# Performance work log

Measured on AMD Instinct MI355X. Metric: run time of the kernel, lower is better.

The kernel has to match this reference:

```python
import jax, jax.numpy as jnp
import numpy as np
import math

K = 8
MOMENTUM = 0.999


def _gelu(x):
    c = math.sqrt(2.0 / math.pi)
    return 0.5 * x * (1.0 + jnp.tanh(c * (x + 0.044715 * x ** 3)))


def _normalize(v, eps=1e-12):
    n = jnp.linalg.norm(v, axis=-1, keepdims=True)
    return v / jnp.maximum(n, eps)


def setup_inputs() -> dict:
    key = jax.random.key(0)
    k1, k2 = jax.random.split(key)
    B, T, D = 4, 4096, 2048
    x = jax.random.normal(k1, (B, T, D), dtype=jnp.float32)
    prototypes = _normalize(jax.random.normal(k2, (K, D), dtype=jnp.float32))
    log_tau = jnp.asarray(math.log(2.0), dtype=jnp.float32)
    log_blend = jnp.asarray(math.log(0.3 / 0.7), dtype=jnp.float32)
    return {"x": x, "prototypes": prototypes, "log_tau": log_tau, "log_blend": log_blend}


def reference(x, prototypes, log_tau, log_blend):
    tau = jnp.exp(log_tau)
    alpha = jax.nn.sigmoid(log_blend)
    B, T, D = x.shape
    x_flat = jax.lax.stop_gradient(x.reshape(-1, D))  # [N, D], detached

    P_norm = _normalize(prototypes)                  # [K, D]
    xn = _normalize(x_flat, eps=1e-8)                # [N, D]

    sims = jnp.clip(xn @ P_norm.T, -1.0, 1.0)        # [N, K]
    assignments = jnp.argmax(sims, axis=-1)          # [N]

    # masked per-cluster mean via segment-sum (vectorized over K)
    sums = jax.ops.segment_sum(x_flat, assignments, num_segments=K)       # [K, D]
    counts = jax.ops.segment_sum(jnp.ones((x_flat.shape[0],), x.dtype),
                                 assignments, num_segments=K)             # [K]
    has = (counts > 0)[:, None]
    centroids = jnp.where(has, sums / jnp.maximum(counts, 1.0)[:, None], prototypes)
    new_P = _normalize(centroids)

    P2 = MOMENTUM * prototypes + (1.0 - MOMENTUM) * new_P
    P2n = _normalize(P2, eps=1e-8)

    sims2 = jnp.clip(xn @ P2n.T, -1.0, 1.0)          # [N, K]
    dists = jnp.clip(1.0 - jnp.max(sims2, axis=-1), 0.0, 2.0)
    novelty = (1.0 - jnp.exp(-tau * dists)).reshape(B, T)

    scale = jnp.clip(1.0 - alpha + alpha * novelty[..., None], 0.1, 10.0)
    return _gelu(x * scale)
```

## Files before the change

### kernel.cpp

```cpp
#include <hip/hip_runtime.h>

#define N_TOK 16384
#define DDIM  2048
#define KC    8
#define CH1   32
#define TBA   4
#define TBF   4

typedef float nfloat4 __attribute__((ext_vector_type(4)));

__device__ __forceinline__ void nt_store4(const float4& v, float* p){
  nfloat4 nv; nv.x = v.x; nv.y = v.y; nv.z = v.z; nv.w = v.w;
  __builtin_nontemporal_store(nv, (nfloat4*)p);
}
__device__ __forceinline__ float4 nt_load4(const float* p){
  nfloat4 nv = __builtin_nontemporal_load((const nfloat4*)p);
  return make_float4(nv.x, nv.y, nv.z, nv.w);
}

__device__ __forceinline__ float wave_sum(float v){
  #pragma unroll
  for (int off = 32; off > 0; off >>= 1)
    v += __shfl_xor(v, off, 64);
  return v;
}

__device__ __forceinline__ float butterfly8(float v[8], int t){
  {
    const bool h = (t & 1);
    #pragma unroll
    for (int j = 0; j < 4; ++j){
      float s    = h ? v[j]   : v[j+4];
      float keep = h ? v[j+4] : v[j];
      v[j] = keep + __shfl_xor(s, 1, 64);
    }
  }
  {
    const bool h = (t & 2);
    #pragma unroll
    for (int j = 0; j < 2; ++j){
      float s    = h ? v[j]   : v[j+2];
      float keep = h ? v[j+2] : v[j];
      v[j] = keep + __shfl_xor(s, 2, 64);
    }
  }
  {
    const bool h = (t & 4);
    float s    = h ? v[0] : v[1];
    float keep = h ? v[1] : v[0];
    v[0] = keep + __shfl_xor(s, 4, 64);
  }
  v[0] += __shfl_xor(v[0], 8, 64);
  v[0] += __shfl_xor(v[0], 16, 64);
  v[0] += __shfl_xor(v[0], 32, 64);
  return v[0];
}

__device__ __forceinline__ float gelu_tanh(float v){
  const float c = 0.7978845608028654f;
  float tt = c * v * (1.0f + 0.044715f * v * v);
  float e  = __expf(2.0f * tt);
  float th = 1.0f - 2.0f / (e + 1.0f);
  return 0.5f * v * (1.0f + th);
}

__global__ __launch_bounds__(256, 2)
void k_assign(const float* __restrict__ x, const float* __restrict__ proto,
              float* __restrict__ psums, float* __restrict__ pcnts, int ntok)
{
  const int t = threadIdx.x;
  const int wave = t >> 6, lane = t & 63;
  const int d0 = 4*t, d1 = DDIM/2 + 4*t;
  const int kidx = ((lane&1)<<2) | (lane&2) | ((lane>>2)&1);

  __shared__ float rednorm[4*KC];
  __shared__ float red[TBA][4][KC];
  __shared__ float sInv[KC];
  __shared__ float sCnt[KC];
  __shared__ int   sAsg[TBA];

  float4 P0[KC], P1[KC];
  float4 acc0[KC], acc1[KC];
  #pragma unroll
  for (int k = 0; k < KC; ++k){
    P0[k] = *(const float4*)(proto + k*DDIM + d0);
    P1[k] = *(const float4*)(proto + k*DDIM + d1);
    acc0[k] = make_float4(0.f,0.f,0.f,0.f);
    acc1[k] = make_float4(0.f,0.f,0.f,0.f);
  }
  if (t < KC) sCnt[t] = 0.f;

  #pragma unroll
  for (int k = 0; k < KC; ++k){
    float ss = P0[k].x*P0[k].x + P0[k].y*P0[k].y + P0[k].z*P0[k].z + P0[k].w*P0[k].w
             + P1[k].x*P1[k].x + P1[k].y*P1[k].y + P1[k].z*P1[k].z + P1[k].w*P1[k].w;
    ss = wave_sum(ss);
    if (lane == 0) rednorm[wave*KC + k] = ss;
  }
  __syncthreads();
  if (t < KC){
    float ss = rednorm[t] + rednorm[KC + t] + rednorm[2*KC + t] + rednorm[3*KC + t];
    sInv[t] = 1.0f / fmaxf(sqrtf(ss), 1e-12f);
  }
  __syncthreads();

  const int stride = gridDim.x * TBA;
  float4 X0[TBA], X1[TBA], N0[TBA], N1[TBA];
  int tok0 = blockIdx.x * TBA;
  #pragma unroll
  for (int i = 0; i < TBA; ++i){
    int tk = tok0 + i;
    X0[i] = make_float4(0,0,0,0); X1[i] = make_float4(0,0,0,0);
    if (tk < ntok){
      X0[i] = *(const float4*)(x + (size_t)tk*DDIM + d0);
      X1[i] = *(const float4*)(x + (size_t)tk*DDIM + d1);
    }
  }

  for (; tok0 < ntok; tok0 += stride){
    const int ntok0 = tok0 + stride;
    #pragma unroll
    for (int i = 0; i < TBA; ++i){
      int tk = ntok0 + i;
      N0[i] = make_float4(0,0,0,0); N1[i] = make_float4(0,0,0,0);
      if (tk < ntok){
        N0[i] = *(const float4*)(x + (size_t)tk*DDIM + d0);
        N1[i] = *(const float4*)(x + (size_t)tk*DDIM + d1);
      }
    }
    #pragma unroll
    for (int i = 0; i < TBA; ++i){
      float v[KC];
      #pragma unroll
      for (int k = 0; k < KC; ++k){
        v[k] = X0[i].x*P0[k].x + X0[i].y*P0[k].y + X0[i].z*P0[k].z + X0[i].w*P0[k].w
             + X1[i].x*P1[k].x + X1[i].y*P1[k].y + X1[i].z*P1[k].z + X1[i].w*P1[k].w;
      }
      float r = butterfly8(v, t);
      if (lane < 8) red[i][wave][kidx] = r;
    }
    __syncthreads();
    if (t < TBA && tok0 + t < ntok){
      int best = 0; float bv = -3.4e38f;
      #pragma unroll
      for (int k = 0; k < KC; ++k){
        float val = (red[t][0][k] + red[t][1][k] + red[t][2][k] + red[t][3][k]) * sInv[k];
        if (val > bv){ bv = val; best = k; }
      }
      sAsg[t] = best;
      atomicAdd(&sCnt[best], 1.0f);
    }
    __syncthreads();
    #pragma unroll
    for (int i = 0; i < TBA; ++i){
      if (tok0 + i < ntok){
        const int a = sAsg[i];
        #pragma unroll
        for (int k = 0; k < KC; ++k){
          if (a == k){
            acc0[k].x += X0[i].x; acc0[k].y += X0[i].y; acc0[k].z += X0[i].z; acc0[k].w += X0[i].w;
            acc1[k].x += X1[i].x; acc1[k].y += X1[i].y; acc1[k].z += X1[i].z; acc1[k].w += X1[i].w;
          }
        }
      }
    }
    #pragma unroll
    for (int i = 0; i < TBA; ++i){ X0[i] = N0[i]; X1[i] = N1[i]; }
  }
  __syncthreads();
  float* dst = psums + (size_t)blockIdx.x * (KC*DDIM);
  #pragma unroll
  for (int k = 0; k < KC; ++k){
    nt_store4(acc0[k], dst + k*DDIM + d0);
    nt_store4(acc1[k], dst + k*DDIM + d1);
  }
  if (t < KC) pcnts[blockIdx.x*KC + t] = sCnt[t];
}

__global__ __launch_bounds__(256)
void k_reduce1(const float* __restrict__ psums, const float* __restrict__ pcnts,
               float* __restrict__ stage2, float* __restrict__ cnt2, int nb, int cs)
{
  const int ch = blockIdx.x >> 4;
  const int g  = blockIdx.x & 15;
  const int col = g*1024 + threadIdx.x*4;
  const int b0 = ch*cs;

  float4 acc = make_float4(0.f,0.f,0.f,0.f);
  #pragma unroll 4
  for (int i = 0; i < cs; ++i){
    int b = b0 + i;
    if (b < nb){
      float4 v = nt_load4(psums + (size_t)b*(KC*DDIM) + col);
      acc.x += v.x; acc.y += v.y; acc.z += v.z; acc.w += v.w;
    }
  }
  *(float4*)(stage2 + (size_t)ch*(KC*DDIM) + col) = acc;

  if (g == 0 && threadIdx.x < KC){
    float c = 0.f;
    for (int i = 0; i < cs; ++i){
      int b = b0 + i;
      if (b < nb) c += pcnts[b*KC + threadIdx.x];
    }
    cnt2[ch*KC + threadIdx.x] = c;
  }
}

__global__ __launch_bounds__(256)
void k_reduce2(const float* __restrict__ stage2, const float* __restrict__ cnt2,
               const float* __restrict__ proto, float* __restrict__ centroid)
{
  __shared__ float cnt[KC];
  if (threadIdx.x < KC){
    float c = 0.f;
    #pragma unroll
    for (int ch = 0; ch < CH1; ++ch) c += cnt2[ch*KC + threadIdx.x];
    cnt[threadIdx.x] = c;
  }
  __syncthreads();
  const int col = blockIdx.x*1024 + threadIdx.x*4;
  float4 s = make_float4(0.f,0.f,0.f,0.f);
  #pragma unroll
  for (int ch = 0; ch < CH1; ++ch){
    float4 v = *(const float4*)(stage2 + (size_t)ch*(KC*DDIM) + col);
    s.x += v.x; s.y += v.y; s.z += v.z; s.w += v.w;
  }
  const int k = col >> 11;
  const float c = cnt[k];
  float4 o;
  if (c > 0.f){
    float inv = 1.0f / fmaxf(c, 1.f);
    o.x = s.x*inv; o.y = s.y*inv; o.z = s.z*inv; o.w = s.w*inv;
  } else {
    o = *(const float4*)(proto + col);
  }
  *(float4*)(centroid + col) = o;
}

__global__ void k_pupdate(const float* __restrict__ centroid, const float* __restrict__ proto,
                          float* __restrict__ p2n)
{
  const int t = threadIdx.x;
  const int w = t >> 6, lane = t & 63;
  float4 c[8], pr[8];
  float ss = 0.f;
  #pragma unroll
  for (int j = 0; j < 8; ++j){
    const int d = (j*64 + lane)*4;
    c[j]  = *(const float4*)(centroid + w*DDIM + d);
    pr[j] = *(const float4*)(proto    + w*DDIM + d);
    ss += c[j].x*c[j].x + c[j].y*c[j].y + c[j].z*c[j].z + c[j].w*c[j].w;
  }
  ss = wave_sum(ss);
  const float invc = 1.0f / fmaxf(sqrtf(ss), 1e-12f);
  const float m = 0.999f, om = 1.0f - 0.999f;
  float4 p2[8];
  float ss2 = 0.f;
  #pragma unroll
  for (int j = 0; j < 8; ++j){
    p2[j].x = m*pr[j].x + om*c[j].x*invc;
    p2[j].y = m*pr[j].y + om*c[j].y*invc;
    p2[j].z = m*pr[j].z + om*c[j].z*invc;
    p2[j].w = m*pr[j].w + om*c[j].w*invc;
    ss2 += p2[j].x*p2[j].x + p2[j].y*p2[j].y + p2[j].z*p2[j].z + p2[j].w*p2[j].w;
  }
  ss2 = wave_sum(ss2);
  const float inv2 = 1.0f / fmaxf(sqrtf(ss2), 1e-8f);
  #pragma unroll
  for (int j = 0; j < 8; ++j){
    const int d = (j*64 + lane)*4;
    float4 o;
    o.x = p2[j].x*inv2; o.y = p2[j].y*inv2; o.z = p2[j].z*inv2; o.w = p2[j].w*inv2;
    *(float4*)(p2n + w*DDIM + d) = o;
  }
}

__global__ __launch_bounds__(256, 2)
void k_final(const float* __restrict__ x, const float* __restrict__ p2n,
             const float* __restrict__ plog_tau, const float* __restrict__ plog_blend,
             float* __restrict__ out, int ntok)
{
  const int t = threadIdx.x;
  const int wave = t >> 6, lane = t & 63;
  const int d0 = 4*t, d1 = DDIM/2 + 4*t;
  const int kidx = ((lane&1)<<2) | (lane&2) | ((lane>>2)&1);

  __shared__ float red[TBF][4][KC];
  __shared__ float redss[TBF][4];
  __shared__ float sScale[TBF];

  float4 P0[KC], P1[KC];
  #pragma unroll
  for (int k = 0; k < KC; ++k){
    P0[k] = *(const float4*)(p2n + k*DDIM + d0);
    P1[k] = *(const float4*)(p2n + k*DDIM + d1);
  }
  const float tau   = __expf(plog_tau[0]);
  const float alpha = 1.0f / (1.0f + __expf(-plog_blend[0]));

  const int stride = gridDim.x * TBF;
  float4 X0[TBF], X1[TBF], N0[TBF], N1[TBF];
  int tok0 = blockIdx.x * TBF;
  #pragma unroll
  for (int i = 0; i < TBF; ++i){
    int tk = tok0 + i;
    X0[i] = make_float4(0,0,0,0); X1[i] = make_float4(0,0,0,0);
    if (tk < ntok){
      X0[i] = *(const float4*)(x + (size_t)tk*DDIM + d0);
      X1[i] = *(const float4*)(x + (size_t)tk*DDIM + d1);
    }
  }

  for (; tok0 < ntok; tok0 += stride){
    const int ntok0 = tok0 + stride;
    #pragma unroll
    for (int i = 0; i < TBF; ++i){
      int tk = ntok0 + i;
      N0[i] = make_float4(0,0,0,0); N1[i] = make_float4(0,0,0,0);
      if (tk < ntok){
        N0[i] = *(const float4*)(x + (size_t)tk*DDIM + d0);
        N1[i] = *(const float4*)(x + (size_t)tk*DDIM + d1);
      }
    }
    #pragma unroll
    for (int i = 0; i < TBF; ++i){
      float v[KC];
      #pragma unroll
      for (int k = 0; k < KC; ++k){
        v[k] = X0[i].x*P0[k].x + X0[i].y*P0[k].y + X0[i].z*P0[k].z + X0[i].w*P0[k].w
             + X1[i].x*P1[k].x + X1[i].y*P1[k].y + X1[i].z*P1[k].z + X1[i].w*P1[k].w;
      }
      float r = butterfly8(v, t);
      if (lane < 8) red[i][wave][kidx] = r;
      float ss = X0[i].x*X0[i].x + X0[i].y*X0[i].y + X0[i].z*X0[i].z + X0[i].w*X0[i].w
               + X1[i].x*X1[i].x + X1[i].y*X1[i].y + X1[i].z*X1[i].z + X1[i].w*X1[i].w;
      ss = wave_sum(ss);
      if (lane == 0) redss[i][wave] = ss;
    }
    __syncthreads();
    if (t < TBF && tok0 + t < ntok){
      float fss = redss[t][0] + redss[t][1] + redss[t][2] + redss[t][3];
      float inv = 1.0f / fmaxf(sqrtf(fss), 1e-8f);
      float mx = -3.4e38f;
      #pragma unroll
      for (int k = 0; k < KC; ++k){
        float val = red[t][0][k] + red[t][1][k] + red[t][2][k] + red[t][3][k];
        mx = fmaxf(mx, val);
      }
      float s    = fminf(fmaxf(mx * inv, -1.0f), 1.0f);
      float dist = fminf(fmaxf(1.0f - s, 0.0f), 2.0f);
      float nov  = 1.0f - __expf(-tau * dist);
      float sc   = 1.0f - alpha + alpha * nov;
      sScale[t]  = fminf(fmaxf(sc, 0.1f), 10.0f);
    }
    __syncthreads();
    #pragma unroll
    for (int i = 0; i < TBF; ++i){
      int tk = tok0 + i;
      if (tk < ntok){
        const float sc = sScale[i];
        float* o = out + (size_t)tk*DDIM;
        float4 o0, o1;
        o0.x = gelu_tanh(X0[i].x*sc); o0.y = gelu_tanh(X0[i].y*sc);
        o0.z = gelu_tanh(X0[i].z*sc); o0.w = gelu_tanh(X0[i].w*sc);
        o1.x = gelu_tanh(X1[i].x*sc); o1.y = gelu_tanh(X1[i].y*sc);
        o1.z = gelu_tanh(X1[i].z*sc); o1.w = gelu_tanh(X1[i].w*sc);
        nt_store4(o0, o + d0);
        nt_store4(o1, o + d1);
      }
    }
    #pragma unroll
    for (int i = 0; i < TBF; ++i){ X0[i] = N0[i]; X1[i] = N1[i]; }
  }
}

extern "C" void kernel_launch(void* const* d_in, const int* in_sizes, int n_in,
                              void* d_out, int out_size, void* d_ws, size_t ws_size,
                              hipStream_t stream)
{
  const float* x          = (const float*)d_in[0];
  const float* proto      = (const float*)d_in[1];
  const float* log_tau    = (const float*)d_in[2];
  const float* log_blend  = (const float*)d_in[3];
  float* out = (float*)d_out;
  float* ws  = (float*)d_ws;

  const int ntok = in_sizes[0] / DDIM;

  float* centroid = ws;
  float* p2n      = ws + 16384;
  float* pcnts    = ws + 32768;
  float* cnt2     = ws + 36864;
  float* stage2   = ws + 37120;
  float* psums    = ws + 37120 + CH1*KC*DDIM;

  long cap = (long)(ws_size / 4) - (37120 + CH1*KC*DDIM);
  int nb = (int)(cap / (KC * DDIM));
  if (nb > 512) nb = 512;
  if (nb < 1)  nb = 1;
  const int cs = (nb + CH1 - 1) / CH1;

  k_assign <<<nb,      256, 0, stream>>>(x, proto, psums, pcnts, ntok);
  k_reduce1<<<CH1*16,  256, 0, stream>>>(psums, pcnts, stage2, cnt2, nb, cs);
  k_reduce2<<<16,      256, 0, stream>>>(stage2, cnt2, proto, centroid);
  k_pupdate<<<1,       512, 0, stream>>>(centroid, proto, p2n);
  k_final  <<<512,     256, 0, stream>>>(x, p2n, log_tau, log_blend, out, ntok);
}
```

Before: 308.0 us.

## Restructure pipeline with bf16 prototypes in LDS, per-wave tokens, bf16 partial sums

Reworks the whole pipeline. Prototypes are pre-normalized and stored as bf16 in shared memory, and each wave handles whole tokens with in-wave argmax, which removes the per-token block syncs. Per-block partial sums are written as bf16 and the centroid and prototype updates are merged into one kernel. Grids are now one block per 16 tokens instead of a persistent grid. The bf16 prototypes and partial sums can change the argmax for near-tied tokens and lose accuracy in the sums, and the partial buffer grows to about 1024 blocks.

```diff
diff --git a/kernel.cpp b/kernel.cpp
--- a/kernel.cpp
+++ b/kernel.cpp
@@ -1,22 +1,30 @@
 #include <hip/hip_runtime.h>
 
-#define N_TOK 16384
 #define DDIM  2048
 #define KC    8
-#define CH1   32
-#define TBA   4
-#define TBF   4
+#define NCH   32
+#define TPB_A 16
+#define TPB_C 16
 
 typedef float nfloat4 __attribute__((ext_vector_type(4)));
+typedef unsigned short ushortv8 __attribute__((ext_vector_type(8)));
+typedef unsigned short ushortv4 __attribute__((ext_vector_type(4)));
 
 __device__ __forceinline__ void nt_store4(const float4& v, float* p){
   nfloat4 nv; nv.x = v.x; nv.y = v.y; nv.z = v.z; nv.w = v.w;
   __builtin_nontemporal_store(nv, (nfloat4*)p);
 }
-__device__ __forceinline__ float4 nt_load4(const float* p){
-  nfloat4 nv = __builtin_nontemporal_load((const nfloat4*)p);
-  return make_float4(nv.x, nv.y, nv.z, nv.w);
-}
+
+__device__ __forceinline__ unsigned short f2bf(float f){
+  unsigned u = __float_as_uint(f);
+  u += 0x7fffu + ((u >> 16) & 1u);
+  return (unsigned short)(u >> 16);
+}
+__device__ __forceinline__ float bf2f(unsigned short h){
+  return __uint_as_float(((unsigned)h) << 16);
+}
+__device__ __forceinline__ float bflo(unsigned u){ return __uint_as_float(u << 16); }
+__device__ __forceinline__ float bfhi(unsigned u){ return __uint_as_float(u & 0xffff0000u); }
 
 __device__ __forceinline__ float wave_sum(float v){
   #pragma unroll
@@ -64,314 +72,317 @@
   return 0.5f * v * (1.0f + th);
 }
 
-__global__ __launch_bounds__(256, 2)
-void k_assign(const float* __restrict__ x, const float* __restrict__ proto,
-              float* __restrict__ psums, float* __restrict__ pcnts, int ntok)
-{
+__global__ __launch_bounds__(256)
+void k_pre(const float* __restrict__ proto, unsigned short* __restrict__ pbf)
+{
+  const int k = blockIdx.x, t = threadIdx.x;
+  const int wave = t >> 6, lane = t & 63;
+  __shared__ float sred[4];
+  const int d0 = 4*t, d1 = 1024 + 4*t;
+  float4 a = *(const float4*)(proto + k*DDIM + d0);
+  float4 b = *(const float4*)(proto + k*DDIM + d1);
+  float ss = a.x*a.x + a.y*a.y + a.z*a.z + a.w*a.w
+           + b.x*b.x + b.y*b.y + b.z*b.z + b.w*b.w;
+  ss = wave_sum(ss);
+  if (lane == 0) sred[wave] = ss;
+  __syncthreads();
+  ss = sred[0] + sred[1] + sred[2] + sred[3];
+  const float inv = 1.0f / fmaxf(sqrtf(ss), 1e-12f);
+  ushortv4 o0, o1;
+  o0[0]=f2bf(a.x*inv); o0[1]=f2bf(a.y*inv); o0[2]=f2bf(a.z*inv); o0[3]=f2bf(a.w*inv);
+  o1[0]=f2bf(b.x*inv); o1[1]=f2bf(b.y*inv); o1[2]=f2bf(b.z*inv); o1[3]=f2bf(b.w*inv);
+  *(ushortv4*)(pbf + k*DDIM + d0) = o0;
+  *(ushortv4*)(pbf + k*DDIM + d1) = o1;
+}
+
+__global__ __launch_bounds__(256, 4)
+void k_assign(const float* __restrict__ x, const unsigned short* __restrict__ pbf,
+              unsigned short* __restrict__ part, float* __restrict__ pcnts, int ntok)
+{
+  __shared__ unsigned short Pl[KC*DDIM];
+  __shared__ int asg[TPB_A];
+
   const int t = threadIdx.x;
   const int wave = t >> 6, lane = t & 63;
-  const int d0 = 4*t, d1 = DDIM/2 + 4*t;
-  const int kidx = ((lane&1)<<2) | (lane&2) | ((lane>>2)&1);
-
-  __shared__ float rednorm[4*KC];
-  __shared__ float red[TBA][4][KC];
-  __shared__ float sInv[KC];
-  __shared__ float sCnt[KC];
-  __shared__ int   sAsg[TBA];
-
-  float4 P0[KC], P1[KC];
+
+  #pragma unroll
+  for (int j = 0; j < 8; ++j){
+    const int e = (j*256 + t)*8;
+    *(ushortv8*)(Pl + e) = *(const ushortv8*)(pbf + e);
+  }
+  __syncthreads();
+
+  const int tok_base = blockIdx.x * TPB_A;
+
+  {
+    const int tl0 = wave*4;
+    float4 X[8], N[8];
+    int tok = tok_base + tl0;
+    if (tok < ntok){
+      #pragma unroll
+      for (int j = 0; j < 8; ++j)
+        X[j] = *(const float4*)(x + (size_t)tok*DDIM + j*256 + 4*lane);
+    }
+    #pragma unroll
+    for (int i = 0; i < 4; ++i){
+      const int tok_i = tok_base + tl0 + i;
+      const bool ldn = (i < 3) && (tok_i + 1 < ntok);
+      if (ldn){
+        #pragma unroll
+        for (int j = 0; j < 8; ++j)
+          N[j] = *(const float4*)(x + (size_t)(tok_i+1)*DDIM + j*256 + 4*lane);
+      }
+      if (tok_i < ntok){
+        float v[KC];
+        #pragma unroll
+        for (int k = 0; k < KC; ++k){
+          float s = 0.f;
+          #pragma unroll
+          for (int j = 0; j < 8; ++j){
+            uint2 u = *(const uint2*)((const unsigned*)Pl + k*1024 + j*128 + 2*lane);
+            s += X[j].x*bflo(u.x) + X[j].y*bfhi(u.x)
+               + X[j].z*bflo(u.y) + X[j].w*bfhi(u.y);
+          }
+          v[k] = s;
+        }
+        float bv = butterfly8(v, lane);
+        int   bi = ((lane&1)<<2) | (lane&2) | ((lane>>2)&1);
+        #pragma unroll
+        for (int off = 1; off < 8; off <<= 1){
+          float ov = __shfl_xor(bv, off, 64);
+          int   oi = __shfl_xor(bi, off, 64);
+          if (ov > bv || (ov == bv && oi < bi)){ bv = ov; bi = oi; }
+        }
+        if (lane == 0) asg[tl0 + i] = bi;
+      }
+      if (ldn){
+        #pragma unroll
+        for (int j = 0; j < 8; ++j) X[j] = N[j];
+      }
+    }
+  }
+  __syncthreads();
+
+  const int d0 = 4*t, d1 = 1024 + 4*t;
   float4 acc0[KC], acc1[KC];
+  float cnt[KC];
   #pragma unroll
   for (int k = 0; k < KC; ++k){
-    P0[k] = *(const float4*)(proto + k*DDIM + d0);
-    P1[k] = *(const float4*)(proto + k*DDIM + d1);
     acc0[k] = make_float4(0.f,0.f,0.f,0.f);
     acc1[k] = make_float4(0.f,0.f,0.f,0.f);
-  }
-  if (t < KC) sCnt[t] = 0.f;
-
+    cnt[k] = 0.f;
+  }
+  #pragma unroll
+  for (int i = 0; i < TPB_A; ++i){
+    const int tok = tok_base + i;
+    if (tok < ntok){
+      const int a = __builtin_amdgcn_readfirstlane(asg[i]);
+      float4 xa = *(const float4*)(x + (size_t)tok*DDIM + d0);
+      float4 xb = *(const float4*)(x + (size_t)tok*DDIM + d1);
+      #pragma unroll
+      for (int k = 0; k < KC; ++k){
+        if (a == k){
+          acc0[k].x += xa.x; acc0[k].y += xa.y; acc0[k].z += xa.z; acc0[k].w += xa.w;
+          acc1[k].x += xb.x; acc1[k].y += xb.y; acc1[k].z += xb.z; acc1[k].w += xb.w;
+          cnt[k] += 1.f;
+        }
+      }
+    }
+  }
+  unsigned short* dst = part + (size_t)blockIdx.x * (KC*DDIM);
   #pragma unroll
   for (int k = 0; k < KC; ++k){
-    float ss = P0[k].x*P0[k].x + P0[k].y*P0[k].y + P0[k].z*P0[k].z + P0[k].w*P0[k].w
-             + P1[k].x*P1[k].x + P1[k].y*P1[k].y + P1[k].z*P1[k].z + P1[k].w*P1[k].w;
-    ss = wave_sum(ss);
-    if (lane == 0) rednorm[wave*KC + k] = ss;
-  }
-  __syncthreads();
-  if (t < KC){
-    float ss = rednorm[t] + rednorm[KC + t] + rednorm[2*KC + t] + rednorm[3*KC + t];
-    sInv[t] = 1.0f / fmaxf(sqrtf(ss), 1e-12f);
-  }
-  __syncthreads();
-
-  const int stride = gridDim.x * TBA;
-  float4 X0[TBA], X1[TBA], N0[TBA], N1[TBA];
-  int tok0 = blockIdx.x * TBA;
-  #pragma unroll
-  for (int i = 0; i < TBA; ++i){
-    int tk = tok0 + i;
-    X0[i] = make_float4(0,0,0,0); X1[i] = make_float4(0,0,0,0);
-    if (tk < ntok){
-      X0[i] = *(const float4*)(x + (size_t)tk*DDIM + d0);
-      X1[i] = *(const float4*)(x + (size_t)tk*DDIM + d1);
-    }
-  }
-
-  for (; tok0 < ntok; tok0 += stride){
-    const int ntok0 = tok0 + stride;
+    ushortv4 o0, o1;
+    o0[0]=f2bf(acc0[k].x); o0[1]=f2bf(acc0[k].y); o0[2]=f2bf(acc0[k].z); o0[3]=f2bf(acc0[k].w);
+    o1[0]=f2bf(acc1[k].x); o1[1]=f2bf(acc1[k].y); o1[2]=f2bf(acc1[k].z); o1[3]=f2bf(acc1[k].w);
+    *(ushortv4*)(dst + k*DDIM + d0) = o0;
+    *(ushortv4*)(dst + k*DDIM + d1) = o1;
+  }
+  if (t == 0){
     #pragma unroll
-    for (int i = 0; i < TBA; ++i){
-      int tk = ntok0 + i;
-      N0[i] = make_float4(0,0,0,0); N1[i] = make_float4(0,0,0,0);
-      if (tk < ntok){
-        N0[i] = *(const float4*)(x + (size_t)tk*DDIM + d0);
-        N1[i] = *(const float4*)(x + (size_t)tk*DDIM + d1);
-      }
-    }
-    #pragma unroll
-    for (int i = 0; i < TBA; ++i){
-      float v[KC];
-      #pragma unroll
-      for (int k = 0; k < KC; ++k){
-        v[k] = X0[i].x*P0[k].x + X0[i].y*P0[k].y + X0[i].z*P0[k].z + X0[i].w*P0[k].w
-             + X1[i].x*P1[k].x + X1[i].y*P1[k].y + X1[i].z*P1[k].z + X1[i].w*P1[k].w;
-      }
-      float r = butterfly8(v, t);
-      if (lane < 8) red[i][wave][kidx] = r;
-    }
-    __syncthreads();
-    if (t < TBA && tok0 + t < ntok){
-      int best = 0; float bv = -3.4e38f;
-      #pragma unroll
-      for (int k = 0; k < KC; ++k){
-        float val = (red[t][0][k] + red[t][1][k] + red[t][2][k] + red[t][3][k]) * sInv[k];
-        if (val > bv){ bv = val; best = k; }
-      }
-      sAsg[t] = best;
-      atomicAdd(&sCnt[best], 1.0f);
-    }
-    __syncthreads();
-    #pragma unroll
-    for (int i = 0; i < TBA; ++i){
-      if (tok0 + i < ntok){
-        const int a = sAsg[i];
-        #pragma unroll
-        for (int k = 0; k < KC; ++k){
-          if (a == k){
-            acc0[k].x += X0[i].x; acc0[k].y += X0[i].y; acc0[k].z += X0[i].z; acc0[k].w += X0[i].w;
-            acc1[k].x += X1[i].x; acc1[k].y += X1[i].y; acc1[k].z += X1[i].z; acc1[k].w += X1[i].w;
-          }
-        }
-      }
-    }
-    #pragma unroll
-    for (int i = 0; i < TBA; ++i){ X0[i] = N0[i]; X1[i] = N1[i]; }
-  }
-  __syncthreads();
-  float* dst = psums + (size_t)blockIdx.x * (KC*DDIM);
-  #pragma unroll
-  for (int k = 0; k < KC; ++k){
-    nt_store4(acc0[k], dst + k*DDIM + d0);
-    nt_store4(acc1[k], dst + k*DDIM + d1);
-  }
-  if (t < KC) pcnts[blockIdx.x*KC + t] = sCnt[t];
+    for (int k = 0; k < KC; ++k) pcnts[blockIdx.x*KC + k] = cnt[k];
+  }
 }
 
 __global__ __launch_bounds__(256)
-void k_reduce1(const float* __restrict__ psums, const float* __restrict__ pcnts,
-               float* __restrict__ stage2, float* __restrict__ cnt2, int nb, int cs)
-{
-  const int ch = blockIdx.x >> 4;
-  const int g  = blockIdx.x & 15;
-  const int col = g*1024 + threadIdx.x*4;
+void k_reduce1(const unsigned short* __restrict__ part, const float* __restrict__ pcnts,
+               float* __restrict__ stage2, float* __restrict__ cnt2, int nbA, int cs)
+{
+  const int ch = blockIdx.x >> 3;
+  const int g  = blockIdx.x & 7;
+  const int t  = threadIdx.x;
+  const int col = g*2048 + t*8;
   const int b0 = ch*cs;
 
-  float4 acc = make_float4(0.f,0.f,0.f,0.f);
-  #pragma unroll 4
+  float acc[8] = {0.f,0.f,0.f,0.f,0.f,0.f,0.f,0.f};
   for (int i = 0; i < cs; ++i){
-    int b = b0 + i;
-    if (b < nb){
-      float4 v = nt_load4(psums + (size_t)b*(KC*DDIM) + col);
-      acc.x += v.x; acc.y += v.y; acc.z += v.z; acc.w += v.w;
-    }
-  }
-  *(float4*)(stage2 + (size_t)ch*(KC*DDIM) + col) = acc;
-
-  if (g == 0 && threadIdx.x < KC){
+    const int b = b0 + i;
+    if (b < nbA){
+      ushortv8 v = *(const ushortv8*)(part + (size_t)b*(KC*DDIM) + col);
+      #pragma unroll
+      for (int j = 0; j < 8; ++j) acc[j] += bf2f(v[j]);
+    }
+  }
+  float4 o0 = make_float4(acc[0],acc[1],acc[2],acc[3]);
+  float4 o1 = make_float4(acc[4],acc[5],acc[6],acc[7]);
+  *(float4*)(stage2 + (size_t)ch*(KC*DDIM) + col)     = o0;
+  *(float4*)(stage2 + (size_t)ch*(KC*DDIM) + col + 4) = o1;
+
+  if (g == 0 && t < KC){
     float c = 0.f;
     for (int i = 0; i < cs; ++i){
-      int b = b0 + i;
-      if (b < nb) c += pcnts[b*KC + threadIdx.x];
-    }
-    cnt2[ch*KC + threadIdx.x] = c;
+      const int b = b0 + i;
+      if (b < nbA) c += pcnts[b*KC + t];
+    }
+    cnt2[ch*KC + t] = c;
   }
 }
 
 __global__ __launch_bounds__(256)
-void k_reduce2(const float* __restrict__ stage2, const float* __restrict__ cnt2,
-               const float* __restrict__ proto, float* __restrict__ centroid)
-{
-  __shared__ float cnt[KC];
-  if (threadIdx.x < KC){
-    float c = 0.f;
-    #pragma unroll
-    for (int ch = 0; ch < CH1; ++ch) c += cnt2[ch*KC + threadIdx.x];
-    cnt[threadIdx.x] = c;
-  }
-  __syncthreads();
-  const int col = blockIdx.x*1024 + threadIdx.x*4;
-  float4 s = make_float4(0.f,0.f,0.f,0.f);
-  #pragma unroll
-  for (int ch = 0; ch < CH1; ++ch){
-    float4 v = *(const float4*)(stage2 + (size_t)ch*(KC*DDIM) + col);
-    s.x += v.x; s.y += v.y; s.z += v.z; s.w += v.w;
-  }
-  const int k = col >> 11;
-  const float c = cnt[k];
-  float4 o;
+void k_mid(const float* __restrict__ stage2, const float* __restrict__ cnt2,
+           const float* __restrict__ proto, unsigned short* __restrict__ p2nbf)
+{
+  const int k = blockIdx.x, t = threadIdx.x;
+  const int wave = t >> 6, lane = t & 63;
+  __shared__ float s1[4], s2[4];
+  const int d0 = 4*t, d1 = 1024 + 4*t;
+
+  float4 a = make_float4(0.f,0.f,0.f,0.f), b = make_float4(0.f,0.f,0.f,0.f);
+  #pragma unroll
+  for (int ch = 0; ch < NCH; ++ch){
+    const float* p = stage2 + (size_t)ch*(KC*DDIM) + k*DDIM;
+    float4 u = *(const float4*)(p + d0);
+    float4 w = *(const float4*)(p + d1);
+    a.x += u.x; a.y += u.y; a.z += u.z; a.w += u.w;
+    b.x += w.x; b.y += w.y; b.z += w.z; b.w += w.w;
+  }
+  float c = 0.f;
+  #pragma unroll
+  for (int ch = 0; ch < NCH; ++ch) c += cnt2[ch*KC + k];
+
+  float4 pr0 = *(const float4*)(proto + k*DDIM + d0);
+  float4 pr1 = *(const float4*)(proto + k*DDIM + d1);
+
+  float4 c0, c1;
   if (c > 0.f){
-    float inv = 1.0f / fmaxf(c, 1.f);
-    o.x = s.x*inv; o.y = s.y*inv; o.z = s.z*inv; o.w = s.w*inv;
-  } else {
-    o = *(const float4*)(proto + col);
-  }
-  *(float4*)(centroid + col) = o;
-}
-
-__global__ void k_pupdate(const float* __restrict__ centroid, const float* __restrict__ proto,
-                          float* __restrict__ p2n)
-{
-  const int t = threadIdx.x;
-  const int w = t >> 6, lane = t & 63;
-  float4 c[8], pr[8];
-  float ss = 0.f;
-  #pragma unroll
-  for (int j = 0; j < 8; ++j){
-    const int d = (j*64 + lane)*4;
-    c[j]  = *(const float4*)(centroid + w*DDIM + d);
-    pr[j] = *(const float4*)(proto    + w*DDIM + d);
-    ss += c[j].x*c[j].x + c[j].y*c[j].y + c[j].z*c[j].z + c[j].w*c[j].w;
-  }
+    const float inv = 1.0f / fmaxf(c, 1.0f);
+    c0.x=a.x*inv; c0.y=a.y*inv; c0.z=a.z*inv; c0.w=a.w*inv;
+    c1.x=b.x*inv; c1.y=b.y*inv; c1.z=b.z*inv; c1.w=b.w*inv;
+  } else { c0 = pr0; c1 = pr1; }
+
+  float ss = c0.x*c0.x + c0.y*c0.y + c0.z*c0.z + c0.w*c0.w
+           + c1.x*c1.x + c1.y*c1.y + c1.z*c1.z + c1.w*c1.w;
   ss = wave_sum(ss);
+  if (lane == 0) s1[wave] = ss;
+  __syncthreads();
+  ss = s1[0] + s1[1] + s1[2] + s1[3];
   const float invc = 1.0f / fmaxf(sqrtf(ss), 1e-12f);
+
   const float m = 0.999f, om = 1.0f - 0.999f;
-  float4 p2[8];
-  float ss2 = 0.f;
-  #pragma unroll
-  for (int j = 0; j < 8; ++j){
-    p2[j].x = m*pr[j].x + om*c[j].x*invc;
-    p2[j].y = m*pr[j].y + om*c[j].y*invc;
-    p2[j].z = m*pr[j].z + om*c[j].z*invc;
-    p2[j].w = m*pr[j].w + om*c[j].w*invc;
-    ss2 += p2[j].x*p2[j].x + p2[j].y*p2[j].y + p2[j].z*p2[j].z + p2[j].w*p2[j].w;
-  }
+  float4 p20, p21;
+  p20.x = m*pr0.x + om*c0.x*invc; p20.y = m*pr0.y + om*c0.y*invc;
+  p20.z = m*pr0.z + om*c0.z*invc; p20.w = m*pr0.w + om*c0.w*invc;
+  p21.x = m*pr1.x + om*c1.x*invc; p21.y = m*pr1.y + om*c1.y*invc;
+  p21.z = m*pr1.z + om*c1.z*invc; p21.w = m*pr1.w + om*c1.w*invc;
+
+  float ss2 = p20.x*p20.x + p20.y*p20.y + p20.z*p20.z + p20.w*p20.w
+            + p21.x*p21.x + p21.y*p21.y + p21.z*p21.z + p21.w*p21.w;
   ss2 = wave_sum(ss2);
+  if (lane == 0) s2[wave] = ss2;
+  __syncthreads();
+  ss2 = s2[0] + s2[1] + s2[2] + s2[3];
   const float inv2 = 1.0f / fmaxf(sqrtf(ss2), 1e-8f);
-  #pragma unroll
-  for (int j = 0; j < 8; ++j){
-    const int d = (j*64 + lane)*4;
-    float4 o;
-    o.x = p2[j].x*inv2; o.y = p2[j].y*inv2; o.z = p2[j].z*inv2; o.w = p2[j].w*inv2;
-    *(float4*)(p2n + w*DDIM + d) = o;
-  }
-}
-
-__global__ __launch_bounds__(256, 2)
-void k_final(const float* __restrict__ x, const float* __restrict__ p2n,
-             const float* __restrict__ plog_tau, const float* __restrict__ plog_blend,
+
+  ushortv4 o0, o1;
+  o0[0]=f2bf(p20.x*inv2); o0[1]=f2bf(p20.y*inv2); o0[2]=f2bf(p20.z*inv2); o0[3]=f2bf(p20.w*inv2);
+  o1[0]=f2bf(p21.x*inv2); o1[1]=f2bf(p21.y*inv2); o1[2]=f2bf(p21.z*inv2); o1[3]=f2bf(p21.w*inv2);
+  *(ushortv4*)(p2nbf + k*DDIM + d0) = o0;
+  *(ushortv4*)(p2nbf + k*DDIM + d1) = o1;
+}
+
+__global__ __launch_bounds__(256, 4)
+void k_final(const float* __restrict__ x, const unsigned short* __restrict__ p2nbf,
+             const float* __restrict__ plt, const float* __restrict__ plb,
              float* __restrict__ out, int ntok)
 {
+  __shared__ unsigned short Pl[KC*DDIM];
   const int t = threadIdx.x;
   const int wave = t >> 6, lane = t & 63;
-  const int d0 = 4*t, d1 = DDIM/2 + 4*t;
-  const int kidx = ((lane&1)<<2) | (lane&2) | ((lane>>2)&1);
-
-  __shared__ float red[TBF][4][KC];
-  __shared__ float redss[TBF][4];
-  __shared__ float sScale[TBF];
-
-  float4 P0[KC], P1[KC];
-  #pragma unroll
-  for (int k = 0; k < KC; ++k){
-    P0[k] = *(const float4*)(p2n + k*DDIM + d0);
-    P1[k] = *(const float4*)(p2n + k*DDIM + d1);
-  }
-  const float tau   = __expf(plog_tau[0]);
-  const float alpha = 1.0f / (1.0f + __expf(-plog_blend[0]));
-
-  const int stride = gridDim.x * TBF;
-  float4 X0[TBF], X1[TBF], N0[TBF], N1[TBF];
-  int tok0 = blockIdx.x * TBF;
-  #pragma unroll
-  for (int i = 0; i < TBF; ++i){
-    int tk = tok0 + i;
-    X0[i] = make_float4(0,0,0,0); X1[i] = make_float4(0,0,0,0);
-    if (tk < ntok){
-      X0[i] = *(const float4*)(x + (size_t)tk*DDIM + d0);
-      X1[i] = *(const float4*)(x + (size_t)tk*DDIM + d1);
-    }
-  }
-
-  for (; tok0 < ntok; tok0 += stride){
-    const int ntok0 = tok0 + stride;
-    #pragma unroll
-    for (int i = 0; i < TBF; ++i){
-      int tk = ntok0 + i;
-      N0[i] = make_float4(0,0,0,0); N1[i] = make_float4(0,0,0,0);
-      if (tk < ntok){
-        N0[i] = *(const float4*)(x + (size_t)tk*DDIM + d0);
-        N1[i] = *(const float4*)(x + (size_t)tk*DDIM + d1);
-      }
-    }
-    #pragma unroll
-    for (int i = 0; i < TBF; ++i){
+
+  #pragma unroll
+  for (int j = 0; j < 8; ++j){
+    const int e = (j*256 + t)*8;
+    *(ushortv8*)(Pl + e) = *(const ushortv8*)(p2nbf + e);
+  }
+  __syncthreads();
+
+  const float tau   = __expf(plt[0]);
+  const float alpha = 1.0f / (1.0f + __expf(-plb[0]));
+
+  const int tl0 = wave*4;
+  const int tok_base = blockIdx.x * TPB_C;
+  float4 X[8], N[8];
+  {
+    const int tok = tok_base + tl0;
+    if (tok < ntok){
+      #pragma unroll
+      for (int j = 0; j < 8; ++j)
+        X[j] = *(const float4*)(x + (size_t)tok*DDIM + j*256 + 4*lane);
+    }
+  }
+  #pragma unroll
+  for (int i = 0; i < 4; ++i){
+    const int tok_i = tok_base + tl0 + i;
+    const bool ldn = (i < 3) && (tok_i + 1 < ntok);
+    if (ldn){
+      #pragma unroll
+      for (int j = 0; j < 8; ++j)
+        N[j] = *(const float4*)(x + (size_t)(tok_i+1)*DDIM + j*256 + 4*lane);
+    }
+    if (tok_i < ntok){
+      float ss = 0.f;
+      #pragma unroll
+      for (int j = 0; j < 8; ++j)
+        ss += X[j].x*X[j].x + X[j].y*X[j].y + X[j].z*X[j].z + X[j].w*X[j].w;
+      ss = wave_sum(ss);
+
       float v[KC];
       #pragma unroll
       for (int k = 0; k < KC; ++k){
-        v[k] = X0[i].x*P0[k].x + X0[i].y*P0[k].y + X0[i].z*P0[k].z + X0[i].w*P0[k].w
-             + X1[i].x*P1[k].x + X1[i].y*P1[k].y + X1[i].z*P1[k].z + X1[i].w*P1[k].w;
-      }
-      float r = butterfly8(v, t);
-      if (lane < 8) red[i][wave][kidx] = r;
-      float ss = X0[i].x*X0[i].x + X0[i].y*X0[i].y + X0[i].z*X0[i].z + X0[i].w*X0[i].w
-               + X1[i].x*X1[i].x + X1[i].y*X1[i].y + X1[i].z*X1[i].z + X1[i].w*X1[i].w;
-      ss = wave_sum(ss);
-      if (lane == 0) redss[i][wave] = ss;
-    }
-    __syncthreads();
-    if (t < TBF && tok0 + t < ntok){
-      float fss = redss[t][0] + redss[t][1] + redss[t][2] + redss[t][3];
-      float inv = 1.0f / fmaxf(sqrtf(fss), 1e-8f);
-      float mx = -3.4e38f;
-      #pragma unroll
-      for (int k = 0; k < KC; ++k){
-        float val = red[t][0][k] + red[t][1][k] + red[t][2][k] + red[t][3][k];
-        mx = fmaxf(mx, val);
-      }
-      float s    = fminf(fmaxf(mx * inv, -1.0f), 1.0f);
-      float dist = fminf(fmaxf(1.0f - s, 0.0f), 2.0f);
-      float nov  = 1.0f - __expf(-tau * dist);
-      float sc   = 1.0f - alpha + alpha * nov;
-      sScale[t]  = fminf(fmaxf(sc, 0.1f), 10.0f);
-    }
-    __syncthreads();
-    #pragma unroll
-    for (int i = 0; i < TBF; ++i){
-      int tk = tok0 + i;
-      if (tk < ntok){
-        const float sc = sScale[i];
-        float* o = out + (size_t)tk*DDIM;
-        float4 o0, o1;
-        o0.x = gelu_tanh(X0[i].x*sc); o0.y = gelu_tanh(X0[i].y*sc);
-        o0.z = gelu_tanh(X0[i].z*sc); o0.w = gelu_tanh(X0[i].w*sc);
-        o1.x = gelu_tanh(X1[i].x*sc); o1.y = gelu_tanh(X1[i].y*sc);
-        o1.z = gelu_tanh(X1[i].z*sc); o1.w = gelu_tanh(X1[i].w*sc);
-        nt_store4(o0, o + d0);
-        nt_store4(o1, o + d1);
-      }
-    }
-    #pragma unroll
-    for (int i = 0; i < TBF; ++i){ X0[i] = N0[i]; X1[i] = N1[i]; }
+        float s = 0.f;
+        #pragma unroll
+        for (int j = 0; j < 8; ++j){
+          uint2 u = *(const uint2*)((const unsigned*)Pl + k*1024 + j*128 + 2*lane);
+          s += X[j].x*bflo(u.x) + X[j].y*bfhi(u.x)
+             + X[j].z*bflo(u.y) + X[j].w*bfhi(u.y);
+        }
+        v[k] = s;
+      }
+      float mx = butterfly8(v, lane);
+      mx = fmaxf(mx, __shfl_xor(mx, 1, 64));
+      mx = fmaxf(mx, __shfl_xor(mx, 2, 64));
+      mx = fmaxf(mx, __shfl_xor(mx, 4, 64));
+
+      const float inv  = 1.0f / fmaxf(sqrtf(ss), 1e-8f);
+      const float s    = fminf(fmaxf(mx * inv, -1.0f), 1.0f);
+      const float dist = fminf(fmaxf(1.0f - s, 0.0f), 2.0f);
+      const float nov  = 1.0f - __expf(-tau * dist);
+      float sc = 1.0f - alpha + alpha * nov;
+      sc = fminf(fmaxf(sc, 0.1f), 10.0f);
+
+      float* o = out + (size_t)tok_i*DDIM;
+      #pragma unroll
+      for (int j = 0; j < 8; ++j){
+        float4 g;
+        g.x = gelu_tanh(X[j].x*sc); g.y = gelu_tanh(X[j].y*sc);
+        g.z = gelu_tanh(X[j].z*sc); g.w = gelu_tanh(X[j].w*sc);
+        nt_store4(g, o + j*256 + 4*lane);
+      }
+    }
+    if (ldn){
+      #pragma unroll
+      for (int j = 0; j < 8; ++j) X[j] = N[j];
+    }
   }
 }
 
@@ -379,31 +390,29 @@
                               void* d_out, int out_size, void* d_ws, size_t ws_size,
                               hipStream_t stream)
 {
-  const float* x          = (const float*)d_in[0];
-  const float* proto      = (const float*)d_in[1];
-  const float* log_tau    = (const float*)d_in[2];
-  const float* log_blend  = (const float*)d_in[3];
+  const float* x         = (const float*)d_in[0];
+  const float* proto     = (const float*)d_in[1];
+  const float* log_tau   = (const float*)d_in[2];
+  const float* log_blend = (const float*)d_in[3];
   float* out = (float*)d_out;
   float* ws  = (float*)d_ws;
 
   const int ntok = in_sizes[0] / DDIM;
 
-  float* centroid = ws;
-  float* p2n      = ws + 16384;
-  float* pcnts    = ws + 32768;
-  float* cnt2     = ws + 36864;
-  float* stage2   = ws + 37120;
-  float* psums    = ws + 37120 + CH1*KC*DDIM;
-
-  long cap = (long)(ws_size / 4) - (37120 + CH1*KC*DDIM);
-  int nb = (int)(cap / (KC * DDIM));
-  if (nb > 512) nb = 512;
-  if (nb < 1)  nb = 1;
-  const int cs = (nb + CH1 - 1) / CH1;
-
-  k_assign <<<nb,      256, 0, stream>>>(x, proto, psums, pcnts, ntok);
-  k_reduce1<<<CH1*16,  256, 0, stream>>>(psums, pcnts, stage2, cnt2, nb, cs);
-  k_reduce2<<<16,      256, 0, stream>>>(stage2, cnt2, proto, centroid);
-  k_pupdate<<<1,       512, 0, stream>>>(centroid, proto, p2n);
-  k_final  <<<512,     256, 0, stream>>>(x, p2n, log_tau, log_blend, out, ntok);
-}
+  unsigned short* pbf    = (unsigned short*)(ws);
+  unsigned short* p2nbf  = (unsigned short*)(ws + 8192);
+  float*          pcnts  = ws + 16384;
+  float*          cnt2   = ws + 24576;
+  float*          stage2 = ws + 24832;
+  unsigned short* part   = (unsigned short*)(ws + 549120);
+
+  const int nbA = (ntok + TPB_A - 1) / TPB_A;
+  const int nbC = (ntok + TPB_C - 1) / TPB_C;
+  const int cs  = (nbA + NCH - 1) / NCH;
+
+  k_pre    <<<KC,     256, 0, stream>>>(proto, pbf);
+  k_assign <<<nbA,    256, 0, stream>>>(x, pbf, part, pcnts, ntok);
+  k_reduce1<<<NCH*8,  256, 0, stream>>>(part, pcnts, stage2, cnt2, nbA, cs);
+  k_mid    <<<KC,     256, 0, stream>>>(stage2, cnt2, proto, p2nbf);
+  k_final  <<<nbC,    256, 0, stream>>>(x, p2nbf, log_tau, log_blend, out, ntok);
+}
```

After: 306.4 us. About the same (-0.5%).
